# Kernel tuning notes

Hardware: AMD Instinct MI355X
Metric: run time of the kernel (lower is better)

The kernel has to match this reference:

```python
import jax, jax.numpy as jnp
import numpy as np

RATIOS = np.array([0.5, 1.0, 2.0], np.float32)
SCALES = np.array([8.0, 16.0, 32.0], np.float32)
IMAGE_SIZE = 1920.0
UPPER, LOWER = 0.4, 0.1
NPOS_MAX, NNEG_MAX = 128, 60   # sample_num=256 -> bg_num = min(60, 256-npos) = 60
BETA = 0.1
EPS = 1e-6


def make_anchors(H, W, stride):
    # K = len(RATIOS)*len(SCALES) anchors per grid cell, sizes stride*scale, aspect per ratio
    ws = (stride * SCALES[None, :] * np.sqrt(1.0 / RATIOS[:, None])).reshape(-1)  # [K]
    hs = (stride * SCALES[None, :] * np.sqrt(RATIOS[:, None])).reshape(-1)        # [K]
    cx = (np.arange(W, dtype=np.float32) + 0.5) * stride
    cy = (np.arange(H, dtype=np.float32) + 0.5) * stride
    cxg, cyg = np.meshgrid(cx, cy)  # [H, W]
    a = np.stack([cxg[..., None] - ws / 2, cyg[..., None] - hs / 2,
                  cxg[..., None] + ws / 2, cyg[..., None] + hs / 2], axis=-1)  # [H, W, K, 4]
    return jnp.asarray(a, jnp.float32)


def pairwise_iou(b, g):
    # b: [A, 4], g: [M, 4] -> [A, M]
    ab = jnp.maximum(b[:, 2] - b[:, 0], 0.0) * jnp.maximum(b[:, 3] - b[:, 1], 0.0)
    ag = jnp.maximum(g[:, 2] - g[:, 0], 0.0) * jnp.maximum(g[:, 3] - g[:, 1], 0.0)
    x1 = jnp.maximum(b[:, None, 0], g[None, :, 0])
    y1 = jnp.maximum(b[:, None, 1], g[None, :, 1])
    x2 = jnp.minimum(b[:, None, 2], g[None, :, 2])
    y2 = jnp.minimum(b[:, None, 3], g[None, :, 3])
    inter = jnp.maximum(x2 - x1, 0.0) * jnp.maximum(y2 - y1, 0.0)
    return inter / (ab[:, None] + ag[None, :] - inter + EPS)


def encode(box, anchor):
    # standard (tx, ty, tw, th) box encoding relative to anchor
    aw = anchor[:, 2] - anchor[:, 0]; ah = anchor[:, 3] - anchor[:, 1]
    acx = anchor[:, 0] + 0.5 * aw; acy = anchor[:, 1] + 0.5 * ah
    bw = jnp.maximum(box[:, 2] - box[:, 0], EPS); bh = jnp.maximum(box[:, 3] - box[:, 1], EPS)
    bcx = box[:, 0] + 0.5 * bw; bcy = box[:, 1] + 0.5 * bh
    return jnp.stack([(bcx - acx) / aw, (bcy - acy) / ah,
                      jnp.log(bw / aw), jnp.log(bh / ah)], axis=-1)


def smooth_l1(d):
    ad = jnp.abs(d)
    return jnp.where(ad < BETA, 0.5 * d * d / BETA, ad - 0.5 * BETA)


def per_image(regions, cls, gt, key, anchors_flat, n_norm):
    iou = pairwise_iou(regions, gt)                       # [A, M]
    best = iou.max(axis=1)
    arg = iou.argmax(axis=1).astype(jnp.int32)
    # match(): >= upper -> gt index (positive), < lower -> NEGATIVE(-1), else ignore(-2)
    matches = jnp.where(best >= UPPER, arg, jnp.where(best < LOWER, -1, -2))
    kp, kn = jax.random.split(key)
    # randperm-style sampling without replacement: top_k over random scores on masked anchors
    pos_score = jnp.where(matches >= 0, jax.random.uniform(kp, matches.shape), -1.0)
    pv, pidx = jax.lax.top_k(pos_score, NPOS_MAX)
    pvalid = (pv > 0.0).astype(jnp.float32)               # npos = min(num_pos, 128)
    neg_score = jnp.where(matches == -1, jax.random.uniform(kn, matches.shape), -1.0)
    nv, nidx = jax.lax.top_k(neg_score, NNEG_MAX)
    nvalid = (nv > 0.0).astype(jnp.float32)
    npos = pvalid.sum(); nneg = nvalid.sum()
    lp = cls[pidx]; ln = cls[nidx]
    # BCEWithLogits(mean): label 1 -> softplus(-x), label 0 -> softplus(x)
    bce = jnp.sum(jax.nn.softplus(-lp) * pvalid) + jnp.sum(jax.nn.softplus(ln) * nvalid)
    denom = jnp.maximum(npos + nneg, 1.0)
    cls_loss = bce / denom
    gt_sel = gt[jnp.clip(matches[pidx], 0, gt.shape[0] - 1)]
    anc = anchors_flat[pidx]
    tp = encode(regions[pidx], anc)
    tg = encode(gt_sel, anc)
    l1 = smooth_l1(tp - tg).sum(-1)                       # [NPOS_MAX]
    bbox_loss = jnp.sum(l1 * pvalid) / (jnp.maximum(npos, 1.0) * n_norm)
    pred_mean = (jnp.sum(lp * pvalid) + jnp.sum(ln * nvalid)) / denom
    return cls_loss, bbox_loss, npos, nneg, pred_mean


def reference(cls_scores, bbox_deltas, gt_boxes):
    N, K, H, W = cls_scores.shape
    stride = round(IMAGE_SIZE / W)
    anc = make_anchors(H, W, stride)                      # [H, W, K, 4]
    deltas = bbox_deltas.transpose(0, 2, 3, 1).reshape(N, H, W, K, 4)
    # regions = anchors + deltas, cross_boundary(remove=False) -> clip to image
    regions = jnp.clip(anc[None] + deltas, 0.0, IMAGE_SIZE).reshape(N, -1, 4)
    cls = cls_scores.transpose(0, 2, 3, 1).reshape(N, -1)
    keys = jax.random.split(jax.random.key(42), N)
    cl, bl, fg, bg, pm = jax.vmap(per_image, in_axes=(0, 0, 0, 0, None, None))(
        regions, cls, gt_boxes, keys, anc.reshape(-1, 4), float(N))
    return (cl.sum(), bl.sum(), bg.sum(), fg.sum(), pm[-1])


def setup_inputs():
    key = jax.random.key(0)
    k1, k2, k3, k4 = jax.random.split(key, 4)
    N, K, H, W, M = 8, 9, 120, 120, 64
    cls_scores = jax.random.normal(k1, (N, K, H, W), jnp.float32)
    bbox_deltas = jax.random.normal(k2, (N, 4 * K, H, W), jnp.float32) * 4.0
    xy = jax.random.uniform(k3, (N, M, 2), jnp.float32) * 1500.0
    wh = jax.random.uniform(k4, (N, M, 2), jnp.float32) * 360.0 + 40.0
    gt_boxes = jnp.concatenate([xy, xy + wh], axis=-1)    # valid [x1,y1,x2,y2] in-image
    return {"cls_scores": cls_scores, "bbox_deltas": bbox_deltas, "gt_boxes": gt_boxes}
```

## Files before the change

kernel.cpp:

```cpp
#include <hip/hip_runtime.h>
#include <stdint.h>

#define N_IMG 8
#define K_ANC 9
#define HW_G  14400
#define W_G   120
#define A_TOT 129600
#define M_GT  64
#define NBIN  1024
#define CAP   2048
#define WIN_TOT 2025
#define NBLK_M 1013
#define NSUB2 64

#define POISON_U32 0xAAAAAAAAu

static constexpr size_t OFF_PHIST = 0;
static constexpr size_t OFF_NHIST = 32768;
static constexpr size_t OFF_CNT   = 65536;
static constexpr size_t OFF_THR   = 65600;
static constexpr size_t OFF_DONE  = 65856;
static constexpr size_t OFF_DONE_F= 65888;
static constexpr size_t OFF_ACC   = 65920;
static constexpr size_t OFF_ENT   = 67584;
static constexpr size_t OFF_BND   = OFF_ENT + 4ull * N_IMG * A_TOT;

__device__ __forceinline__ uint32_t rotl32(uint32_t v, int r) {
  return (v << r) | (v >> (32 - r));
}

__device__ void tf2x32(uint32_t k0, uint32_t k1, uint32_t x0, uint32_t x1,
                       uint32_t& o0, uint32_t& o1) {
  uint32_t ks2 = 0x1BD11BDAu ^ k0 ^ k1;
  x0 += k0; x1 += k1;
#define TF_R(r) { x0 += x1; x1 = rotl32(x1, r); x1 ^= x0; }
  TF_R(13) TF_R(15) TF_R(26) TF_R(6)
  x0 += k1; x1 += ks2 + 1u;
  TF_R(17) TF_R(29) TF_R(16) TF_R(24)
  x0 += ks2; x1 += k0 + 2u;
  TF_R(13) TF_R(15) TF_R(26) TF_R(6)
  x0 += k0; x1 += k1 + 3u;
  TF_R(17) TF_R(29) TF_R(16) TF_R(24)
  x0 += k1; x1 += ks2 + 4u;
  TF_R(13) TF_R(15) TF_R(26) TF_R(6)
  x0 += ks2; x1 += k0 + 5u;
#undef TF_R
  o0 = x0; o1 = x1;
}

constexpr uint64_t tf_c(uint32_t k0, uint32_t k1, uint32_t x0, uint32_t x1) {
  const int R[20] = {13,15,26,6,17,29,16,24,13,15,26,6,17,29,16,24,13,15,26,6};
  uint32_t ks[3] = {k0, k1, 0x1BD11BDAu ^ k0 ^ k1};
  x0 += k0; x1 += k1;
  for (int r = 0; r < 20; ++r) {
    x0 += x1; x1 = (x1 << R[r]) | (x1 >> (32 - R[r])); x1 ^= x0;
    if ((r & 3) == 3) {
      int d = r / 4 + 1;
      x0 += ks[d % 3]; x1 += ks[(d + 1) % 3] + (uint32_t)d;
    }
  }
  return ((uint64_t)x0 << 32) | x1;
}

struct KeyTab { uint32_t v[N_IMG][4]; };
constexpr KeyTab make_keys() {
  KeyTab K{};
  for (int n = 0; n < N_IMG; ++n) {
    uint64_t f = tf_c(0u, 42u, 0u, (uint32_t)n);
    uint32_t i0 = (uint32_t)(f >> 32), i1 = (uint32_t)f;
    uint64_t p = tf_c(i0, i1, 0u, 0u);
    uint64_t q = tf_c(i0, i1, 0u, 1u);
    K.v[n][0] = (uint32_t)(p >> 32); K.v[n][1] = (uint32_t)p;
    K.v[n][2] = (uint32_t)(q >> 32); K.v[n][3] = (uint32_t)q;
  }
  return K;
}
__constant__ KeyTab KEYS = make_keys();

__device__ __forceinline__ float rlanef(float v, int l) {
  return __int_as_float(__builtin_amdgcn_readlane(__float_as_int(v), l));
}

__device__ void acc_pos(int n, int l, int m, const float* __restrict__ cls,
                        const float* __restrict__ del, const float* __restrict__ gt,
                        float& sp, float& pr, float& l1s) {
  int k = l / HW_G, hw = l - k * HW_G;
  const float scales[3] = {8.f, 16.f, 32.f};
  const float ratios[3] = {0.5f, 1.f, 2.f};
  float sc = scales[k % 3], rt = ratios[k / 3];
  float wsz = (16.f * sc) * sqrtf(1.f / rt);
  float hsz = (16.f * sc) * sqrtf(rt);
  int w = hw % W_G, h = hw / W_G;
  float cx = ((float)w + 0.5f) * 16.f, cy = ((float)h + 0.5f) * 16.f;
  float ax1 = cx - wsz * 0.5f, ay1 = cy - hsz * 0.5f;
  float ax2 = cx + wsz * 0.5f, ay2 = cy + hsz * 0.5f;
  int base = (n * 36 + k * 4) * HW_G + hw;
  float rx1 = fminf(fmaxf(ax1 + del[base], 0.f), 1920.f);
  float ry1 = fminf(fmaxf(ay1 + del[base + HW_G], 0.f), 1920.f);
  float rx2 = fminf(fmaxf(ax2 + del[base + 2 * HW_G], 0.f), 1920.f);
  float ry2 = fminf(fmaxf(ay2 + del[base + 3 * HW_G], 0.f), 1920.f);
  float L = cls[n * A_TOT + l];
  sp += fmaxf(-L, 0.f) + log1pf(expf(-fabsf(L)));
  pr += L;
  const float* g = gt + (n * M_GT + m) * 4;
  float aw = ax2 - ax1, ah = ay2 - ay1;
  float acx = ax1 + 0.5f * aw, acy = ay1 + 0.5f * ah;
  float bw = fmaxf(rx2 - rx1, 1e-6f), bh = fmaxf(ry2 - ry1, 1e-6f);
  float bcx = rx1 + 0.5f * bw, bcy = ry1 + 0.5f * bh;
  float gw = fmaxf(g[2] - g[0], 1e-6f), gh = fmaxf(g[3] - g[1], 1e-6f);
  float gcx = g[0] + 0.5f * gw, gcy = g[1] + 0.5f * gh;
  float dd[4];
  dd[0] = (bcx - acx) / aw - (gcx - acx) / aw;
  dd[1] = (bcy - acy) / ah - (gcy - acy) / ah;
  dd[2] = logf(bw / aw) - logf(gw / aw);
  dd[3] = logf(bh / ah) - logf(gh / ah);
  float t = 0.f;
  for (int i = 0; i < 4; ++i) {
    float ad = fabsf(dd[i]);
    t += (ad < 0.1f) ? (0.5f * dd[i] * dd[i] / 0.1f) : (ad - 0.05f);
  }
  l1s += t;
}

__device__ void acc_neg(int n, int l, const float* __restrict__ cls,
                        float& sp, float& pr) {
  float L = cls[n * A_TOT + l];
  sp += fmaxf(L, 0.f) + log1pf(expf(-fabsf(L)));
  pr += L;
}

__device__ void reduce3_atomic(float sp, float pr, float l1, float* accf, int n,
                               int tid) {
  __shared__ float swv[3][4];
  float v0 = sp, v1 = pr, v2 = l1;
  for (int off = 32; off > 0; off >>= 1) {
    v0 += __shfl_down(v0, off); v1 += __shfl_down(v1, off); v2 += __shfl_down(v2, off);
  }
  int wv = tid >> 6, ln = tid & 63;
  if (ln == 0) { swv[0][wv] = v0; swv[1][wv] = v1; swv[2][wv] = v2; }
  __syncthreads();
  if (tid == 0) {
    atomicAdd(&accf[n * 48 + 0],  swv[0][0] + swv[0][1] + swv[0][2] + swv[0][3]);
    atomicAdd(&accf[n * 48 + 16], swv[1][0] + swv[1][1] + swv[1][2] + swv[1][3]);
    atomicAdd(&accf[n * 48 + 32], swv[2][0] + swv[2][1] + swv[2][2] + swv[2][3]);
  }
  __syncthreads();
}

__global__ __launch_bounds__(128) void k_match(
    const float* __restrict__ del, const float* __restrict__ gt, uint8_t* ws) {
  const int n = blockIdx.y;
  const int tid = threadIdx.x;
  const int ln = tid & 63;
  const int win = blockIdx.x * 2 + (tid >> 6);
  if (win >= WIN_TOT) return;
  const int k = win / 225;
  const int hw = (win - k * 225) * 64 + ln;

  float4 g4 = reinterpret_cast<const float4*>(gt)[n * M_GT + ln];
  float garea = fmaxf(g4.z - g4.x, 0.f) * fmaxf(g4.w - g4.y, 0.f);

  const float scales[3] = {8.f, 16.f, 32.f};
  const float ratios[3] = {0.5f, 1.f, 2.f};
  float sc = scales[k % 3], rt = ratios[k / 3];
  float wsz = (16.f * sc) * sqrtf(1.f / rt);
  float hsz = (16.f * sc) * sqrtf(rt);
  int w = hw % W_G, h = hw / W_G;
  float cx = ((float)w + 0.5f) * 16.f, cy = ((float)h + 0.5f) * 16.f;
  float ax1 = cx - wsz * 0.5f, ay1 = cy - hsz * 0.5f;
  float ax2 = cx + wsz * 0.5f, ay2 = cy + hsz * 0.5f;
  const float* dp = del + (size_t)(n * 36 + k * 4) * HW_G + hw;
  float rx1 = fminf(fmaxf(ax1 + dp[0], 0.f), 1920.f);
  float ry1 = fminf(fmaxf(ay1 + dp[HW_G], 0.f), 1920.f);
  float rx2 = fminf(fmaxf(ax2 + dp[2 * HW_G], 0.f), 1920.f);
  float ry2 = fminf(fmaxf(ay2 + dp[3 * HW_G], 0.f), 1920.f);
  float ab = fmaxf(rx2 - rx1, 0.f) * fmaxf(ry2 - ry1, 0.f);

  float xmn = rx1, xmx = rx2, ymn = ry1, ymx = ry2;
  for (int off = 32; off > 0; off >>= 1) {
    xmn = fminf(xmn, __shfl_xor(xmn, off));
    xmx = fmaxf(xmx, __shfl_xor(xmx, off));
    ymn = fminf(ymn, __shfl_xor(ymn, off));
    ymx = fmaxf(ymx, __shfl_xor(ymx, off));
  }
  bool keep = (g4.x < xmx) && (g4.z > xmn) && (g4.y < ymx) && (g4.w > ymn);
  unsigned long long mk = __ballot(keep);

  float ib = -1.f, ub = 1.f;
  int arg = 0;
  while (mk) {
    int j = __ffsll((unsigned long long)mk) - 1;
    mk &= mk - 1ull;
    float bx1 = rlanef(g4.x, j), by1 = rlanef(g4.y, j);
    float bx2 = rlanef(g4.z, j), by2 = rlanef(g4.w, j);
    float ga  = rlanef(garea, j);
    float ix1 = fmaxf(rx1, bx1), iy1 = fmaxf(ry1, by1);
    float ix2 = fminf(rx2, bx2), iy2 = fminf(ry2, by2);
    float inter = fmaxf(ix2 - ix1, 0.f) * fmaxf(iy2 - iy1, 0.f);
    float u = ab + ga - inter + 1e-6f;
    bool gc = (inter * ub) > (ib * u);
    ib = gc ? inter : ib;
    ub = gc ? u : ub;
    arg = gc ? j : arg;
  }
  float best = ib / ub;
  int m = (best >= 0.4f) ? arg : ((best < 0.1f) ? -1 : -2);

  uint32_t a32 = (uint32_t)(hw * 9 + k);
  uint32_t sk0 = (m >= 0) ? KEYS.v[n][0] : KEYS.v[n][2];
  uint32_t sk1 = (m >= 0) ? KEYS.v[n][1] : KEYS.v[n][3];
  uint32_t y0, y1;
  tf2x32(sk0, sk1, 0u, a32, y0, y1);
  uint32_t bits = (y0 ^ y1) >> 9;

  uint32_t e = 0u;
  if (bits) {
    if (m >= 0)       e = 0x80000000u | ((uint32_t)m << 23) | bits;
    else if (m == -1) e = bits;
  }
  ((uint32_t*)(ws + OFF_ENT))[(size_t)n * A_TOT + (size_t)k * HW_G + hw] = e;
  if (e) {
    uint32_t* hist = (uint32_t*)(ws + OFF_PHIST);
    uint32_t off = (e >> 31) ? 0u : (uint32_t)(N_IMG * NBIN);
    atomicAdd(&hist[off + n * NBIN + (bits >> 13)], 1u);
  }
}

__global__ __launch_bounds__(256) void k_scan_bound(
    const float* __restrict__ cls, const float* __restrict__ del,
    const float* __restrict__ gt, float* __restrict__ out, uint8_t* ws) {
  const int sub = blockIdx.x, n = blockIdx.y;
  const int tid = threadIdx.x;
  const uint32_t* ent = (const uint32_t*)(ws + OFF_ENT);
  uint32_t* cnt = (uint32_t*)(ws + OFF_CNT);
  int* thrg = (int*)(ws + OFF_THR);
  unsigned long long* bnd = (unsigned long long*)(ws + OFF_BND);
  float* accf = (float*)(ws + OFF_ACC);
  uint32_t* done_img = (uint32_t*)(ws + OFF_DONE);
  uint32_t* done_fin = (uint32_t*)(ws + OFF_DONE_F);

  __shared__ unsigned long long sb[CAP];
  __shared__ int tb[2][3];
  __shared__ int sLast, sFin;

  {
    const int wid = tid >> 6, ln = tid & 63;
    if (wid < 2) {
      const int s = wid;
      const uint32_t* hb = (const uint32_t*)(ws + OFF_PHIST) +
                           (s ? (size_t)N_IMG * NBIN : 0) + (size_t)n * NBIN;
      uint32_t hv[16];
      uint32_t ssum = 0u;
#pragma unroll
      for (int i = 0; i < 16; ++i) {
        hv[i] = hb[ln * 16 + i] - POISON_U32; ssum += hv[i];
      }
      uint32_t sfx = ssum;
#pragma unroll
      for (int off = 1; off < 64; off <<= 1) {
        uint32_t v = __shfl_down(sfx, off);
        sfx += (ln + off < 64) ? v : 0u;
      }
      uint32_t total = __shfl(sfx, 0);
      uint32_t ab1 = __shfl_down(sfx, 1);
      uint32_t above = (ln == 63) ? 0u : ab1;
      const uint32_t kk = s ? 60u : 128u;
      if (total < kk) {
        if (ln == 0) { tb[s][0] = -1; tb[s][1] = 0; tb[s][2] = (int)total; }
      } else if (sfx >= kk && above < kk) {
        uint32_t c = above;
        for (int i = 15;; --i) {
          uint32_t hc = hv[i];
          if (c + hc >= kk) {
            tb[s][0] = ln * 16 + i; tb[s][1] = (int)(kk - c); tb[s][2] = (int)kk;
            break;
          }
          c += hc;
        }
      }
    }
    __syncthreads();
  }
  if (sub == 0 && tid == 0) {
    __hip_atomic_store(&thrg[n * 2 + 0], tb[0][2], __ATOMIC_RELAXED,
                       __HIP_MEMORY_SCOPE_AGENT);
    __hip_atomic_store(&thrg[n * 2 + 1], tb[1][2], __ATOMIC_RELAXED,
                       __HIP_MEMORY_SCOPE_AGENT);
  }

  const int bBp = tb[0][0], bBn = tb[1][0];
  float sp = 0.f, pr = 0.f, l1 = 0.f;
  const uint32_t* en = ent + (size_t)n * A_TOT;
#pragma unroll
  for (int it = 0; it < 2; ++it) {
    int l0 = sub * 2048 + it * 1024 + tid * 4;
    if (l0 >= A_TOT) continue;
    uint4 e4 = *reinterpret_cast<const uint4*>(en + l0);
    uint32_t ev[4] = {e4.x, e4.y, e4.z, e4.w};
#pragma unroll
    for (int j = 0; j < 4; ++j) {
      uint32_t e = ev[j];
      if (!e) continue;
      bool isPos = (e >> 31) != 0u;
      int bB = isPos ? bBp : bBn;
      int l = l0 + j;
      uint32_t bits = e & 0x7FFFFFu;
      int bin = (int)(bits >> 13);
      if (bin > bB) {
        if (isPos) acc_pos(n, l, (int)((e >> 23) & 0x3Fu), cls, del, gt, sp, pr, l1);
        else       acc_neg(n, l, cls, sp, pr);
      } else if (bin == bB) {
        int wq = isPos ? 0 : 1;
        int i = (int)(atomicAdd(&cnt[n * 2 + wq], 1u) - POISON_U32);
        if (i < CAP) {
          int k = l / HW_G, hw = l - k * HW_G, a = hw * 9 + k;
          unsigned long long rec =
              ((unsigned long long)bits << 17) | (unsigned)(0x1FFFF - a);
          __hip_atomic_store(&bnd[(size_t)(n * 2 + wq) * CAP + i], rec,
                             __ATOMIC_RELAXED, __HIP_MEMORY_SCOPE_AGENT);
        }
      }
    }
  }
  reduce3_atomic(sp, pr, l1, accf, n, tid);

  if (tid == 0)
    sLast = (atomicAdd(&done_img[n], 1u) == POISON_U32 + NSUB2 - 1u) ? 1 : 0;
  __syncthreads();
  if (!sLast) return;

  float sp2 = 0.f, pr2 = 0.f, l12 = 0.f;
  for (int wq = 0; wq < 2; ++wq) {
    int need = tb[wq][1];
    if (need > 0) {
      __syncthreads();
      uint32_t cm = __hip_atomic_load(&cnt[n * 2 + wq], __ATOMIC_RELAXED,
                                      __HIP_MEMORY_SCOPE_AGENT);
      int m = min((int)(cm - POISON_U32), CAP);
      unsigned long long* bq = bnd + (size_t)(n * 2 + wq) * CAP;
      for (int i = tid; i < m; i += 256)
        sb[i] = __hip_atomic_load(&bq[i], __ATOMIC_RELAXED,
                                  __HIP_MEMORY_SCOPE_AGENT);
      __syncthreads();
      for (int i = tid; i < m; i += 256) {
        unsigned long long key = sb[i];
        int rank = 0;
        for (int j = 0; j < m; ++j) rank += (sb[j] > key) ? 1 : 0;
        if (rank < need) {
          int a = 0x1FFFF - (int)(key & 0x1FFFFull);
          int k = a % 9, hw = a / 9;
          int l = k * HW_G + hw;
          if (wq == 0) {
            uint32_t e = ent[(size_t)n * A_TOT + l];
            acc_pos(n, l, (int)((e >> 23) & 0x3Fu), cls, del, gt, sp2, pr2, l12);
          } else {
            acc_neg(n, l, cls, sp2, pr2);
          }
        }
      }
      __syncthreads();
    }
  }
  reduce3_atomic(sp2, pr2, l12, accf, n, tid);

  if (tid == 0)
    sFin = (atomicAdd(done_fin, 1u) == POISON_U32 + N_IMG - 1u) ? 1 : 0;
  __syncthreads();
  if (!sFin) return;

  if (tid == 0) {
    const float PF = __uint_as_float(POISON_U32);
    float c = 0.f, b = 0.f, fg = 0.f, bg = 0.f, pm = 0.f;
    for (int nn = 0; nn < N_IMG; ++nn) {
      float npos = (float)__hip_atomic_load(&thrg[nn * 2 + 0], __ATOMIC_RELAXED,
                                            __HIP_MEMORY_SCOPE_AGENT);
      float nneg = (float)__hip_atomic_load(&thrg[nn * 2 + 1], __ATOMIC_RELAXED,
                                            __HIP_MEMORY_SCOPE_AGENT);
      float denom = fmaxf(npos + nneg, 1.f);
      float a0 = __hip_atomic_load(&accf[nn * 48 + 0],  __ATOMIC_RELAXED,
                                   __HIP_MEMORY_SCOPE_AGENT);
      float a1 = __hip_atomic_load(&accf[nn * 48 + 16], __ATOMIC_RELAXED,
                                   __HIP_MEMORY_SCOPE_AGENT);
      float a2 = __hip_atomic_load(&accf[nn * 48 + 32], __ATOMIC_RELAXED,
                                   __HIP_MEMORY_SCOPE_AGENT);
      c += (a0 - PF) / denom;
      b += (a2 - PF) / (fmaxf(npos, 1.f) * 8.0f);
      fg += npos; bg += nneg;
      if (nn == N_IMG - 1) pm = (a1 - PF) / denom;
    }
    out[0] = c; out[1] = b; out[2] = bg; out[3] = fg; out[4] = pm;
  }
}

extern "C" void kernel_launch(void* const* d_in, const int* in_sizes, int n_in,
                              void* d_out, int out_size, void* d_ws, size_t ws_size,
                              hipStream_t stream) {
  (void)in_sizes; (void)n_in; (void)out_size; (void)ws_size;
  const float* cls = (const float*)d_in[0];
  const float* del = (const float*)d_in[1];
  const float* gt  = (const float*)d_in[2];
  float* out = (float*)d_out;
  uint8_t* ws = (uint8_t*)d_ws;

  hipLaunchKernelGGL(k_match, dim3(NBLK_M, N_IMG), dim3(128), 0, stream,
                     del, gt, ws);
  hipLaunchKernelGGL(k_scan_bound, dim3(NSUB2, N_IMG), dim3(256), 0, stream,
                     cls, del, gt, out, ws);
}
```

Before: 125.6 us.

## Compact candidate anchors into per-image lists during matching to shrink scan

The match kernel now also appends every positive anchor, and every negative anchor whose random bits fall in the top histogram bins, to compact per-image lists through atomic counters. The second kernel reads these short lists instead of scanning all 129600 entries per image, and keeps a full-scan fallback for when the negative threshold falls below the prefilter bin. The second kernel's grid shrinks from 64 to 8 blocks per image. In exchange, the match kernel does extra global atomics and scattered writes, and the fallback path runs on far fewer blocks.

Result: slower. 289.8 us (+130.7%).

```diff
diff --git a/kernel.cpp b/kernel.cpp
--- a/kernel.cpp
+++ b/kernel.cpp
@@ -9,9 +9,11 @@
 #define M_GT  64
 #define NBIN  1024
 #define CAP   2048
+#define CAPL  131072
+#define B0BIN 960
 #define WIN_TOT 2025
 #define NBLK_M 1013
-#define NSUB2 64
+#define NSUB3 8
 
 #define POISON_U32 0xAAAAAAAAu
 
@@ -19,11 +21,13 @@
 static constexpr size_t OFF_NHIST = 32768;
 static constexpr size_t OFF_CNT   = 65536;
 static constexpr size_t OFF_THR   = 65600;
+static constexpr size_t OFF_LCNT  = 65664;
 static constexpr size_t OFF_DONE  = 65856;
 static constexpr size_t OFF_DONE_F= 65888;
 static constexpr size_t OFF_ACC   = 65920;
 static constexpr size_t OFF_ENT   = 67584;
 static constexpr size_t OFF_BND   = OFF_ENT + 4ull * N_IMG * A_TOT;
+static constexpr size_t OFF_LIST  = OFF_BND + 8ull * N_IMG * 2 * CAP;
 
 __device__ __forceinline__ uint32_t rotl32(uint32_t v, int r) {
   return (v << r) | (v >> (32 - r));
@@ -218,11 +222,24 @@
     if (m >= 0)       e = 0x80000000u | ((uint32_t)m << 23) | bits;
     else if (m == -1) e = bits;
   }
-  ((uint32_t*)(ws + OFF_ENT))[(size_t)n * A_TOT + (size_t)k * HW_G + hw] = e;
+  const int l = k * HW_G + hw;
+  ((uint32_t*)(ws + OFF_ENT))[(size_t)n * A_TOT + l] = e;
   if (e) {
     uint32_t* hist = (uint32_t*)(ws + OFF_PHIST);
     uint32_t off = (e >> 31) ? 0u : (uint32_t)(N_IMG * NBIN);
     atomicAdd(&hist[off + n * NBIN + (bits >> 13)], 1u);
+    uint32_t* lcnt = (uint32_t*)(ws + OFF_LCNT);
+    uint64_t* list = (uint64_t*)(ws + OFF_LIST);
+    if (e >> 31) {
+      uint32_t i = atomicAdd(&lcnt[n * 2 + 0], 1u) - POISON_U32;
+      list[(size_t)(n * 2 + 0) * CAPL + i] =
+          ((uint64_t)bits << 23) | ((uint64_t)((e >> 23) & 0x3Fu) << 17) |
+          (uint64_t)(uint32_t)l;
+    } else if ((bits >> 13) >= (uint32_t)B0BIN) {
+      uint32_t i = atomicAdd(&lcnt[n * 2 + 1], 1u) - POISON_U32;
+      list[(size_t)(n * 2 + 1) * CAPL + i] =
+          ((uint64_t)bits << 23) | (uint64_t)(uint32_t)l;
+    }
   }
 }
 
@@ -233,6 +250,8 @@
   const int tid = threadIdx.x;
   const uint32_t* ent = (const uint32_t*)(ws + OFF_ENT);
   uint32_t* cnt = (uint32_t*)(ws + OFF_CNT);
+  const uint32_t* lcnt = (const uint32_t*)(ws + OFF_LCNT);
+  const uint64_t* list = (const uint64_t*)(ws + OFF_LIST);
   int* thrg = (int*)(ws + OFF_THR);
   unsigned long long* bnd = (unsigned long long*)(ws + OFF_BND);
   float* accf = (float*)(ws + OFF_ACC);
@@ -240,7 +259,7 @@
   uint32_t* done_fin = (uint32_t*)(ws + OFF_DONE_F);
 
   __shared__ unsigned long long sb[CAP];
-  __shared__ int tb[2][3];
+  __shared__ int tb[2][4];
   __shared__ int sLast, sFin;
 
   {
@@ -265,6 +284,7 @@
       uint32_t ab1 = __shfl_down(sfx, 1);
       uint32_t above = (ln == 63) ? 0u : ab1;
       const uint32_t kk = s ? 60u : 128u;
+      if (ln == 0) tb[s][3] = (int)total;
       if (total < kk) {
         if (ln == 0) { tb[s][0] = -1; tb[s][1] = 0; tb[s][2] = (int)total; }
       } else if (sfx >= kk && above < kk) {
@@ -289,43 +309,88 @@
   }
 
   const int bBp = tb[0][0], bBn = tb[1][0];
+  const uint32_t cP = lcnt[n * 2 + 0] - POISON_U32;
+  const uint32_t cN = lcnt[n * 2 + 1] - POISON_U32;
+  const bool fpN = (bBn >= B0BIN) || (bBn == -1 && (int)cN == tb[1][3]);
   float sp = 0.f, pr = 0.f, l1 = 0.f;
-  const uint32_t* en = ent + (size_t)n * A_TOT;
-#pragma unroll
-  for (int it = 0; it < 2; ++it) {
-    int l0 = sub * 2048 + it * 1024 + tid * 4;
-    if (l0 >= A_TOT) continue;
-    uint4 e4 = *reinterpret_cast<const uint4*>(en + l0);
-    uint32_t ev[4] = {e4.x, e4.y, e4.z, e4.w};
-#pragma unroll
-    for (int j = 0; j < 4; ++j) {
-      uint32_t e = ev[j];
-      if (!e) continue;
-      bool isPos = (e >> 31) != 0u;
-      int bB = isPos ? bBp : bBn;
-      int l = l0 + j;
-      uint32_t bits = e & 0x7FFFFFu;
+
+  if (fpN) {
+    const uint64_t* lp = list + (size_t)(n * 2 + 0) * CAPL;
+    for (uint32_t i = (uint32_t)(sub * 256 + tid); i < cP; i += NSUB3 * 256) {
+      uint64_t rec = lp[i];
+      uint32_t bits = (uint32_t)(rec >> 23);
+      int l = (int)(rec & 0x1FFFFu);
       int bin = (int)(bits >> 13);
-      if (bin > bB) {
-        if (isPos) acc_pos(n, l, (int)((e >> 23) & 0x3Fu), cls, del, gt, sp, pr, l1);
-        else       acc_neg(n, l, cls, sp, pr);
-      } else if (bin == bB) {
-        int wq = isPos ? 0 : 1;
-        int i = (int)(atomicAdd(&cnt[n * 2 + wq], 1u) - POISON_U32);
-        if (i < CAP) {
+      if (bin > bBp) {
+        acc_pos(n, l, (int)((rec >> 17) & 0x3Fu), cls, del, gt, sp, pr, l1);
+      } else if (bin == bBp) {
+        uint32_t i2 = atomicAdd(&cnt[n * 2 + 0], 1u) - POISON_U32;
+        if (i2 < CAP) {
           int k = l / HW_G, hw = l - k * HW_G, a = hw * 9 + k;
-          unsigned long long rec =
-              ((unsigned long long)bits << 17) | (unsigned)(0x1FFFF - a);
-          __hip_atomic_store(&bnd[(size_t)(n * 2 + wq) * CAP + i], rec,
+          __hip_atomic_store(&bnd[(size_t)(n * 2 + 0) * CAP + i2],
+                             ((unsigned long long)bits << 17) |
+                                 (unsigned)(0x1FFFF - a),
                              __ATOMIC_RELAXED, __HIP_MEMORY_SCOPE_AGENT);
         }
       }
     }
+    const uint64_t* lq = list + (size_t)(n * 2 + 1) * CAPL;
+    for (uint32_t i = (uint32_t)(sub * 256 + tid); i < cN; i += NSUB3 * 256) {
+      uint64_t rec = lq[i];
+      uint32_t bits = (uint32_t)(rec >> 23);
+      int l = (int)(rec & 0x1FFFFu);
+      int bin = (int)(bits >> 13);
+      if (bin > bBn) {
+        acc_neg(n, l, cls, sp, pr);
+      } else if (bin == bBn) {
+        uint32_t i2 = atomicAdd(&cnt[n * 2 + 1], 1u) - POISON_U32;
+        if (i2 < CAP) {
+          int k = l / HW_G, hw = l - k * HW_G, a = hw * 9 + k;
+          __hip_atomic_store(&bnd[(size_t)(n * 2 + 1) * CAP + i2],
+                             ((unsigned long long)bits << 17) |
+                                 (unsigned)(0x1FFFF - a),
+                             __ATOMIC_RELAXED, __HIP_MEMORY_SCOPE_AGENT);
+        }
+      }
+    }
+  } else {
+    const uint32_t* en = ent + (size_t)n * A_TOT;
+    for (int it = 0; it < 16; ++it) {
+      int l0 = sub * 16384 + it * 1024 + tid * 4;
+      if (l0 >= A_TOT) continue;
+      uint4 e4 = *reinterpret_cast<const uint4*>(en + l0);
+      uint32_t ev[4] = {e4.x, e4.y, e4.z, e4.w};
+#pragma unroll
+      for (int j = 0; j < 4; ++j) {
+        uint32_t e = ev[j];
+        if (!e) continue;
+        bool isPos = (e >> 31) != 0u;
+        int bB = isPos ? bBp : bBn;
+        int l = l0 + j;
+        uint32_t bits = e & 0x7FFFFFu;
+        int bin = (int)(bits >> 13);
+        if (bin > bB) {
+          if (isPos) acc_pos(n, l, (int)((e >> 23) & 0x3Fu), cls, del, gt,
+                             sp, pr, l1);
+          else       acc_neg(n, l, cls, sp, pr);
+        } else if (bin == bB) {
+          int wq = isPos ? 0 : 1;
+          uint32_t i2 = atomicAdd(&cnt[n * 2 + wq], 1u) - POISON_U32;
+          if (i2 < CAP) {
+            int k = l / HW_G, hw = l - k * HW_G, a = hw * 9 + k;
+            __hip_atomic_store(&bnd[(size_t)(n * 2 + wq) * CAP + i2],
+                               ((unsigned long long)bits << 17) |
+                                   (unsigned)(0x1FFFF - a),
+                               __ATOMIC_RELAXED, __HIP_MEMORY_SCOPE_AGENT);
+          }
+        }
+      }
+    }
   }
   reduce3_atomic(sp, pr, l1, accf, n, tid);
 
   if (tid == 0)
-    sLast = (atomicAdd(&done_img[n], 1u) == POISON_U32 + NSUB2 - 1u) ? 1 : 0;
+    sLast = (atomicAdd(&done_img[n], 1u) == POISON_U32 + NSUB3 - 1u) ? 1 : 0;
   __syncthreads();
   if (!sLast) return;
 
@@ -404,6 +469,6 @@
 
   hipLaunchKernelGGL(k_match, dim3(NBLK_M, N_IMG), dim3(128), 0, stream,
                      del, gt, ws);
-  hipLaunchKernelGGL(k_scan_bound, dim3(NSUB2, N_IMG), dim3(256), 0, stream,
+  hipLaunchKernelGGL(k_scan_bound, dim3(NSUB3, N_IMG), dim3(256), 0, stream,
                      cls, del, gt, out, ws);
 }
```
